# Kernel optimization log

Hardware: AMD Instinct MI355X
Metric: run time of the kernel (lower is better)

The kernel has to match this reference:

```python
import jax, jax.numpy as jnp
import numpy as np

T, N, C, S = 1600, 32, 512, 200
BLANK = 0
ALPHA = 0.5
NEG = -1e30  # finite stand-in for -inf (safe for grads)


def setup_inputs() -> dict:
    key = jax.random.key(0)
    k1, k2, k3 = jax.random.split(key, 3)
    # valid log-probabilities (log-softmax over vocab), shape (T, N, C)
    log_probs = jax.nn.log_softmax(jax.random.normal(k1, (T, N, C), jnp.float32), axis=-1)
    # labels in [1, C) so blank=0 never appears in targets
    targets = jax.random.randint(k2, (N, S), 1, C)
    input_lens = jnp.full((N,), T, dtype=jnp.int32)
    target_lens = jax.random.randint(k3, (N,), S // 2, S + 1)
    return {"log_probs": log_probs, "targets": targets,
            "input_lens": input_lens, "target_lens": target_lens}


def _ctc_forward(log_probs, targets, input_lens, target_lens):
    """Per-example CTC negative log-likelihood (reduction='none')."""
    Tt, Nn, Cc = log_probs.shape
    Ss = targets.shape[1]
    L = 2 * Ss + 1  # extended label sequence: blank, l1, blank, l2, ...

    ext = jnp.zeros((Nn, L), dtype=targets.dtype).at[:, 1::2].set(targets)  # (N, L)
    s_idx = jnp.arange(L)
    ext_m2 = jnp.pad(ext, ((0, 0), (2, 0)), constant_values=BLANK)[:, :L]
    # skip transition s-2 -> s allowed only for non-blank labels differing from s-2
    allow_skip = (ext != BLANK) & (ext != ext_m2) & (s_idx >= 2)[None, :]

    emit0 = jnp.take_along_axis(log_probs[0], ext, axis=1)  # (N, L)
    alpha0 = jnp.full((Nn, L), NEG, jnp.float32)
    alpha0 = alpha0.at[:, 0].set(emit0[:, 0])
    alpha0 = alpha0.at[:, 1].set(jnp.where(target_lens >= 1, emit0[:, 1], NEG))

    def step(alpha, xs):
        lp_t, t = xs  # lp_t: (N, C)
        emit = jnp.take_along_axis(lp_t, ext, axis=1)  # (N, L)
        a1 = jnp.pad(alpha, ((0, 0), (1, 0)), constant_values=NEG)[:, :L]
        a2 = jnp.where(allow_skip,
                       jnp.pad(alpha, ((0, 0), (2, 0)), constant_values=NEG)[:, :L],
                       NEG)
        m = jnp.maximum(jnp.maximum(alpha, a1), a2)
        new = m + jnp.log(jnp.exp(alpha - m) + jnp.exp(a1 - m) + jnp.exp(a2 - m)) + emit
        active = (t < input_lens)[:, None]  # freeze trellis past input_len
        return jnp.where(active, new, alpha), None

    alpha, _ = jax.lax.scan(step, alpha0, (log_probs[1:], jnp.arange(1, Tt)))

    idx_last = (2 * target_lens).astype(jnp.int32)  # final blank position
    idx_prev = jnp.maximum(idx_last - 1, 0)  # final label position
    a_last = jnp.take_along_axis(alpha, idx_last[:, None], axis=1)[:, 0]
    a_prev = jnp.where(target_lens > 0,
                       jnp.take_along_axis(alpha, idx_prev[:, None], axis=1)[:, 0],
                       NEG)
    return -jnp.logaddexp(a_last, a_prev)  # (N,)


def reference(log_probs, targets, input_lens, target_lens):
    per_ex = _ctc_forward(log_probs, targets, input_lens, target_lens)
    # zero_infinity=True: zero out infeasible alignments
    per_ex = jnp.where(per_ex < 1e29, per_ex, 0.0)
    norm = jnp.maximum(target_lens.astype(jnp.float32), 1.0) ** ALPHA
    return jnp.mean(per_ex / norm)
```

## Files before the change

### kernel.cpp

```cpp
#include <hip/hip_runtime.h>

#define T_DIM 1600
#define N_DIM 32
#define C_DIM 512
#define S_DIM 200
#define RCP_LN2 1.44269504088896340736f
#define LN2F 0.69314718055994530942f
#define ESENT (-(1 << 28))

static __device__ __forceinline__ float fast_exp2(float x) {
#if __has_builtin(__builtin_amdgcn_exp2f)
    return __builtin_amdgcn_exp2f(x);
#else
    return exp2f(x);
#endif
}

static __device__ __forceinline__ float fast_log2(float x) {
#if __has_builtin(__builtin_amdgcn_logf)
    return __builtin_amdgcn_logf(x);
#else
    return log2f(x);
#endif
}

static __device__ __forceinline__ float dpp_shr1_f(float x) {
    return __int_as_float(__builtin_amdgcn_update_dpp(
        0, __float_as_int(x), 0x138, 0xf, 0xf, false));
}
static __device__ __forceinline__ int dpp_shr1_i(int x, int old0) {
    return __builtin_amdgcn_update_dpp(old0, x, 0x138, 0xf, 0xf, false);
}
static __device__ __forceinline__ int dpp_prefix_max_i(int x) {
    int t;
    t = __builtin_amdgcn_update_dpp(x, x, 0x111, 0xf, 0xf, false); x = (t > x) ? t : x;
    t = __builtin_amdgcn_update_dpp(x, x, 0x112, 0xf, 0xf, false); x = (t > x) ? t : x;
    t = __builtin_amdgcn_update_dpp(x, x, 0x114, 0xf, 0xf, false); x = (t > x) ? t : x;
    t = __builtin_amdgcn_update_dpp(x, x, 0x118, 0xf, 0xf, false); x = (t > x) ? t : x;
    t = __builtin_amdgcn_update_dpp(x, x, 0x142, 0xf, 0xf, false); x = (t > x) ? t : x;
    t = __builtin_amdgcn_update_dpp(x, x, 0x143, 0xf, 0xf, false); x = (t > x) ? t : x;
    return x;
}

static __device__ __forceinline__ void gl_lds16(const float* g, float* l) {
    __builtin_amdgcn_global_load_lds(
        (const __attribute__((address_space(1))) unsigned int*)g,
        (__attribute__((address_space(3))) unsigned int*)l, 16, 0, 0);
}

#define VMWAIT8()  __builtin_amdgcn_s_waitcnt(0x0F78)
#define VMDRAIN()  __builtin_amdgcn_s_waitcnt(0x0F70)
#define PHASE_SYNC() do {                                                     \
        __builtin_amdgcn_sched_barrier(0);                                    \
        __builtin_amdgcn_s_waitcnt(0xC07F);              \
        __builtin_amdgcn_s_barrier();                                         \
        __builtin_amdgcn_sched_barrier(0);                                    \
    } while (0)

__global__ __launch_bounds__(192) void ctc_dp(
    const float* __restrict__ lp, const int* __restrict__ tgts,
    const int* __restrict__ input_lens, const int* __restrict__ target_lens,
    float* __restrict__ out, float* __restrict__ ws)
{
    __shared__ float rows[3][8][C_DIM];
    __shared__ float slab[2][5][8][64];

    const int blk = blockIdx.x;
    const int n = blk >> 1;
    const int role = blk & 1;
    const int tid = threadIdx.x;
    const int wid = tid >> 6;
    const int lane = tid & 63;
    const int* tgt = tgts + n * S_DIM;

    int len = input_lens[n];
    if (len > T_DIM) len = T_DIM;
    const int lenc = (len < 1) ? 1 : len;
    const int tl = target_lens[n];
    const int mid = (lenc + 1) >> 1;
    const int nsb = lenc - mid;
    const int nsteps = (role == 0) ? mid : nsb;
    const int nc = (nsteps + 7) >> 3;

    float* afin_g = ws + 64 + (size_t)n * 1152;
    float* bfin_g = afin_g + 512;
    int* escF_g = (int*)(afin_g + 1024);
    int* escB_g = escF_g + 64;
    int* counter = (int*)ws + n;

    int lab[4];
    float skh[4];
    if (role == 0) {
#pragma unroll
        for (int jj = 0; jj < 4; ++jj) {
            int s = lane * 8 + 2 * jj + 1;
            int i = (s - 1) >> 1;
            int lb = 0;
            float al = 0.0f;
            if (i < S_DIM) {
                lb = tgt[i];
                if (s >= 3 && i >= 1) al = (tgt[i] != tgt[i - 1]) ? 1.0f : 0.0f;
            }
            if (lb < 0 || lb >= C_DIM) lb = 0;
            lab[jj] = lb;
            skh[jj] = al;
        }
    } else {
#pragma unroll
        for (int jj = 0; jj < 4; ++jj) {
            int shat = lane * 8 + 2 * jj + 1;
            int s = 510 - shat;
            int lb = 0;
            float al = 0.0f;
            if (s >= 1 && s <= 399) {
                lb = tgt[(s - 1) >> 1];
                if (s + 2 <= 400) al = (tgt[(s + 1) >> 1] != tgt[(s - 1) >> 1]) ? 1.0f : 0.0f;
            }
            if (lb < 0 || lb >= C_DIM) lb = 0;
            lab[jj] = lb;
            skh[jj] = al;
        }
    }

    const int r0 = (wid == 1) ? 0 : 4;

    auto tmap = [&](int ti) -> int {
        if (role == 0) return ti > mid - 1 ? mid - 1 : ti;
        int t = lenc - 1 - ti;
        return t < 0 ? 0 : t;
    };

#define STAGE(B_, c_) do {                                                    \
        _Pragma("unroll")                                                     \
        for (int rr_ = 0; rr_ < 4; ++rr_) {                                   \
            int r_ = r0 + rr_;                                                \
            int t_ = tmap((c_) * 8 + r_);                                     \
            const float* g_ = lp + ((size_t)t_ * N_DIM + n) * C_DIM + lane*4; \
            gl_lds16(g_,       &rows[(B_)][r_][0]);                           \
            gl_lds16(g_ + 256, &rows[(B_)][r_][256]);                         \
        }                                                                     \
    } while (0)

#define CONV(B_, S_) do {                                                     \
        float v_[20];                                                         \
        _Pragma("unroll")                                                     \
        for (int rr_ = 0; rr_ < 4; ++rr_) {                                   \
            int r_ = r0 + rr_;                                                \
            v_[rr_ * 5 + 0] = rows[(B_)][r_][0];                              \
            v_[rr_ * 5 + 1] = rows[(B_)][r_][lab[0]];                         \
            v_[rr_ * 5 + 2] = rows[(B_)][r_][lab[1]];                         \
            v_[rr_ * 5 + 3] = rows[(B_)][r_][lab[2]];                         \
            v_[rr_ * 5 + 4] = rows[(B_)][r_][lab[3]];                         \
        }                                                                     \
        __builtin_amdgcn_sched_barrier(0);                                    \
        _Pragma("unroll")                                                     \
        for (int rr_ = 0; rr_ < 4; ++rr_) {                                   \
            int r_ = r0 + rr_;                                                \
            _Pragma("unroll")                                                 \
            for (int j_ = 0; j_ < 5; ++j_)                                    \
                slab[(S_)][j_][r_][lane] =                                    \
                    fast_exp2(v_[rr_ * 5 + j_] * RCP_LN2);                    \
        }                                                                     \
    } while (0)

#define BOUNDARY() do {                                                       \
        float lm_ = fmaxf(fmaxf(fmaxf(a0, a1), fmaxf(a2, a3)),                \
                          fmaxf(fmaxf(a4, a5), fmaxf(a6, a7)));               \
        bool nz_ = (lm_ > 0.0f);                                              \
        int kl_ = (int)((__float_as_uint(lm_) >> 23) & 0xffu) - 127;          \
        int prop_ = nz_ ? (E + kl_) : ESENT;                                  \
        int g_ = dpp_prefix_max_i(prop_ + 32 * lane);                         \
        int Efin_ = g_ - 32 * lane;                                           \
        if (nz_) {                                                            \
            int sh_ = E - Efin_;                                              \
            int h1_ = sh_ / 2, h2_ = sh_ - h1_;                               \
            float f_ = fast_exp2((float)h1_), gg_ = fast_exp2((float)h2_);    \
            float fg_ = f_ * gg_;                                             \
            a0 *= fg_; a1 *= fg_; a2 *= fg_; a3 *= fg_;                       \
            a4 *= fg_; a5 *= fg_; a6 *= fg_; a7 *= fg_;                       \
        }                                                                     \
        int Eprev_ = dpp_shr1_i(Efin_, ESENT);                                \
        E = Efin_;                                                            \
        if (lane == 0) {                                                      \
            scale_d = 0.0f;                                                   \
        } else {                                                              \
            int d_ = Eprev_ - Efin_;               \
            scale_d = (d_ < -126) ? 0.0f : fast_exp2((float)d_);              \
        }                                                                     \
    } while (0)

#define CONSUME_F(c8_, S_, FIRST_) do {                                       \
        float q_[40];                                                         \
        _Pragma("unroll")                                                     \
        for (int r_ = 0; r_ < 8; ++r_)                                        \
            _Pragma("unroll")                                                 \
            for (int j_ = 0; j_ < 5; ++j_)                                    \
                q_[r_ * 5 + j_] = slab[(S_)][j_][r_][lane];                   \
        __builtin_amdgcn_sched_barrier(0);                                    \
        _Pragma("unroll")                                                     \
        for (int r_ = 0; r_ < 8; ++r_) {                                      \
            int t_ = (c8_) + r_;                                              \
            if (t_ >= mid) break;                                             \
            float pb_ = q_[r_ * 5 + 0];                                       \
            float p1_ = q_[r_ * 5 + 1];                                       \
            float p3_ = q_[r_ * 5 + 2];                                       \
            float p5_ = q_[r_ * 5 + 3];                                       \
            float p7_ = q_[r_ * 5 + 4];                                       \
            if ((FIRST_) && r_ == 0) {                                        \
                if (lane == 0) {                                              \
                    a0 = pb_;                                                 \
                    a1 = (tl >= 1) ? p1_ : 0.0f;                              \
                }                                                             \
            } else {                                                          \
                float P_ = dpp_shr1_f(a7) * scale_d;                          \
                float n0_ = (a0 + P_) * pb_;                                  \
                float n1_ = fmaf(skh[0], P_,  a1 + a0) * p1_;                 \
                float n2_ = (a2 + a1) * pb_;                                  \
                float n3_ = fmaf(skh[1], a1, a3 + a2) * p3_;                  \
                float n4_ = (a4 + a3) * pb_;                                  \
                float n5_ = fmaf(skh[2], a3, a5 + a4) * p5_;                  \
                float n6_ = (a6 + a5) * pb_;                                  \
                float n7_ = fmaf(skh[3], a5, a7 + a6) * p7_;                  \
                a0 = n0_; a1 = n1_; a2 = n2_; a3 = n3_;                       \
                a4 = n4_; a5 = n5_; a6 = n6_; a7 = n7_;                       \
            }                                                                 \
        }                                                                     \
    } while (0)

#define CONSUME_B(c8_, S_) do {                                               \
        float q_[40];                                                         \
        _Pragma("unroll")                                                     \
        for (int r_ = 0; r_ < 8; ++r_)                                        \
            _Pragma("unroll")                                                 \
            for (int j_ = 0; j_ < 5; ++j_)                                    \
                q_[r_ * 5 + j_] = slab[(S_)][j_][r_][lane];                   \
        __builtin_amdgcn_sched_barrier(0);                                    \
        _Pragma("unroll")                                                     \
        for (int r_ = 0; r_ < 8; ++r_) {                                      \
            int ti_ = (c8_) + r_;                                             \
            if (ti_ >= nsb) break;                                            \
            float pb_ = q_[r_ * 5 + 0];                                       \
            float p1_ = q_[r_ * 5 + 1];                                       \
            float p3_ = q_[r_ * 5 + 2];                                       \
            float p5_ = q_[r_ * 5 + 3];                                       \
            float p7_ = q_[r_ * 5 + 4];                                       \
            float c0_ = pb_ * a0, c1_ = p1_ * a1;                             \
            float c2_ = pb_ * a2, c3_ = p3_ * a3;                             \
            float c4_ = pb_ * a4, c5_ = p5_ * a5;                             \
            float c6_ = pb_ * a6, c7_ = p7_ * a7;                             \
            float P_ = dpp_shr1_f(c7_) * scale_d;                             \
            a0 = c0_ + P_;                                                    \
            a1 = fmaf(skh[0], P_,  c1_ + c0_);                                \
            a2 = c2_ + c1_;                                                   \
            a3 = fmaf(skh[1], c1_, c3_ + c2_);                                \
            a4 = c4_ + c3_;                                                   \
            a5 = fmaf(skh[2], c3_, c5_ + c4_);                                \
            a6 = c6_ + c5_;                                                   \
            a7 = fmaf(skh[3], c5_, c7_ + c6_);                                \
        }                                                                     \
    } while (0)

    if (wid >= 1) {
        STAGE(0, 0);
        STAGE(1, 1);
        VMWAIT8();
        CONV(0, 0);
        STAGE(2, 2);
    }
    PHASE_SYNC();

    float a0, a1, a2, a3, a4, a5, a6, a7;
    if (role == 0) {
        a0 = a1 = a2 = a3 = a4 = a5 = a6 = a7 = 0.0f;
    } else {
#define BINIT(aj_, j_) do {                                                   \
            int s_ = 510 - (lane * 8 + (j_));                                 \
            aj_ = (s_ == 2 * tl || (tl > 0 && s_ == 2 * tl - 1)) ? 1.0f : 0.0f; \
        } while (0)
        BINIT(a0, 0); BINIT(a1, 1); BINIT(a2, 2); BINIT(a3, 3);
        BINIT(a4, 4); BINIT(a5, 5); BINIT(a6, 6); BINIT(a7, 7);
#undef BINIT
    }
    int E = 0;
    float scale_d = (lane == 0) ? 0.0f : 1.0f;

    int bg = 1, bi = 0, sw = 1, sr = 0;
    for (int k = 0; k < nc; ++k) {
        if (wid >= 1) {
            VMWAIT8();
            CONV(bg, sw);
            STAGE(bi, k + 3);
        } else {
            if (role == 0) { CONSUME_F(k * 8, sr, (k == 0)); }
            else           { CONSUME_B(k * 8, sr); }
            BOUNDARY();
        }
        PHASE_SYNC();
        bg = (bg == 2) ? 0 : bg + 1;
        bi = (bi == 2) ? 0 : bi + 1;
        sw ^= 1;
        sr ^= 1;
    }

    if (wid >= 1) {
        VMDRAIN();
        return;
    }

    {
        float4 lo = make_float4(a0, a1, a2, a3);
        float4 hi = make_float4(a4, a5, a6, a7);
        if (role == 0) {
            reinterpret_cast<float4*>(afin_g)[lane * 2] = lo;
            reinterpret_cast<float4*>(afin_g)[lane * 2 + 1] = hi;
            escF_g[lane] = E;
        } else {
            reinterpret_cast<float4*>(bfin_g)[lane * 2] = lo;
            reinterpret_cast<float4*>(bfin_g)[lane * 2 + 1] = hi;
            escB_g[lane] = E;
        }
    }

    __threadfence();
    int prev = 0;
    if (lane == 0)
        prev = __hip_atomic_fetch_add(counter, 1, __ATOMIC_ACQ_REL,
                                      __HIP_MEMORY_SCOPE_AGENT);
    prev = __shfl(prev, 0);
    if (prev != 1) return;

    __threadfence();

    {
        const int l = lane;
        const int Ef = escF_g[l];
        float m8 = -1e30f, s8 = 0.0f;
#pragma unroll
        for (int j = 0; j < 8; ++j) {
            int s = 8 * l + j;
            float x = -1e30f;
            if (s <= 400) {
                float af = afin_g[s];
                int shat = 510 - s;
                float bf = bfin_g[shat];
                if (af > 0.0f && bf > 0.0f)
                    x = fast_log2(af) + fast_log2(bf) + (float)(Ef + escB_g[shat >> 3]);
            }
            float m2 = fmaxf(m8, x);
            s8 = s8 * fast_exp2(m8 - m2) + fast_exp2(x - m2);
            m8 = m2;
        }
        float M = m8, V = s8;
#pragma unroll
        for (int off = 1; off < 64; off <<= 1) {
            float Mo = __shfl_xor(M, off);
            float Vo = __shfl_xor(V, off);
            float Mn = fmaxf(M, Mo);
            V = V * fast_exp2(M - Mn) + Vo * fast_exp2(Mo - Mn);
            M = Mn;
        }
        if (l == 0) {
            float X = M + fast_log2(V);
            float per_ex = -LN2F * X;
            if (!(per_ex < 1e29f)) per_ex = 0.0f;
            float tlf = (float)tl;
            if (tlf < 1.0f) tlf = 1.0f;
            atomicAdd(out, per_ex / sqrtf(tlf) * (1.0f / N_DIM));
        }
    }
#undef STAGE
#undef CONV
#undef BOUNDARY
#undef CONSUME_F
#undef CONSUME_B
}

extern "C" void kernel_launch(void* const* d_in, const int* in_sizes, int n_in,
                              void* d_out, int out_size, void* d_ws, size_t ws_size,
                              hipStream_t stream) {
    (void)in_sizes; (void)n_in; (void)ws_size;
    const float* lp   = (const float*)d_in[0];
    const int* tgts   = (const int*)d_in[1];
    const int* ilens  = (const int*)d_in[2];
    const int* tlens  = (const int*)d_in[3];

    hipMemsetAsync(d_out, 0, (size_t)out_size * sizeof(float), stream);
    hipMemsetAsync(d_ws, 0, N_DIM * sizeof(int), stream);
    ctc_dp<<<2 * N_DIM, 192, 0, stream>>>(lp, tgts, ilens, tlens,
                                          (float*)d_out, (float*)d_ws);
}
```

Before: 230.2 us.

## Split CTC into wide-parallel emission pack kernel plus single-wave DP kernel

Adds a pre-pass kernel, spread over 1024 blocks, that gathers each example's label emissions from every timestep row, exponentiates them, and writes a compact per-(n,t) packed array plus blank probabilities to workspace. The DP kernel then runs as a single wave per role, reading 16-byte packed emissions directly into registers with double-buffered prefetch instead of staging full 512-wide rows through LDS with producer waves and barriers. This takes the gather and exp work off the serial recurrence's critical path. The cost is a second launch and an extra round trip of the packed data through global memory. The old kernel is kept as a fallback when the workspace is too small.

```diff
diff --git a/kernel.cpp b/kernel.cpp
--- a/kernel.cpp
+++ b/kernel.cpp
@@ -27,6 +27,10 @@
 static __device__ __forceinline__ float dpp_shr1_f(float x) {
     return __int_as_float(__builtin_amdgcn_update_dpp(
         0, __float_as_int(x), 0x138, 0xf, 0xf, false));
+}
+static __device__ __forceinline__ float dpp_shl1_f(float x) {
+    return __int_as_float(__builtin_amdgcn_update_dpp(
+        0, __float_as_int(x), 0x130, 0xf, 0xf, false));
 }
 static __device__ __forceinline__ int dpp_shr1_i(int x, int old0) {
     return __builtin_amdgcn_update_dpp(old0, x, 0x138, 0xf, 0xf, false);
@@ -48,29 +52,85 @@
         (__attribute__((address_space(3))) unsigned int*)l, 16, 0, 0);
 }
 
+#define VMWAIT2()  __builtin_amdgcn_s_waitcnt(0x0F72)
 #define VMWAIT8()  __builtin_amdgcn_s_waitcnt(0x0F78)
+#define VMWAIT16() __builtin_amdgcn_s_waitcnt(0x4F70)
 #define VMDRAIN()  __builtin_amdgcn_s_waitcnt(0x0F70)
-#define PHASE_SYNC() do {                                                     \
-        __builtin_amdgcn_sched_barrier(0);                                    \
-        __builtin_amdgcn_s_waitcnt(0xC07F);              \
-        __builtin_amdgcn_s_barrier();                                         \
-        __builtin_amdgcn_sched_barrier(0);                                    \
-    } while (0)
-
-__global__ __launch_bounds__(192) void ctc_dp(
+#define SCHED0()   __builtin_amdgcn_sched_barrier(0)
+
+#define WS_COUNT_F    64
+#define WS_FIN_F      (N_DIM * 1152)
+#define WS_PBL_OFF    (WS_COUNT_F + WS_FIN_F)
+#define WS_PBL_F      (N_DIM * T_DIM + 256)
+#define WS_PACKED_OFF (WS_PBL_OFF + WS_PBL_F)
+#define WS_PACKED_F   ((size_t)N_DIM * T_DIM * 256)
+#define WS_NEED_BYTES (((size_t)WS_PACKED_OFF + WS_PACKED_F) * 4)
+
+__global__ __launch_bounds__(256) void ctc_pack(
     const float* __restrict__ lp, const int* __restrict__ tgts,
+    float* __restrict__ packed, float* __restrict__ pblank)
+{
+    __shared__ float slab[4][2][C_DIM];
+
+    const int wslot = threadIdx.x >> 6;
+    const int lane = threadIdx.x & 63;
+    const int wv = blockIdx.x * 4 + wslot;
+    const int n = wv >> 7;
+    const int w128 = wv & 127;
+    const int* tgt = tgts + n * S_DIM;
+
+    int l0 = 0, l1 = 0, l2 = 0, l3 = 0;
+    if (lane < 50) {
+        int4 li = reinterpret_cast<const int4*>(tgt)[lane];
+        l0 = li.x; l1 = li.y; l2 = li.z; l3 = li.w;
+    }
+    if (l0 < 0 || l0 >= C_DIM) l0 = 0;
+    if (l1 < 0 || l1 >= C_DIM) l1 = 0;
+    if (l2 < 0 || l2 >= C_DIM) l2 = 0;
+    if (l3 < 0 || l3 >= C_DIM) l3 = 0;
+
+    float* sl0 = &slab[wslot][0][0];
+    float* sl1 = &slab[wslot][1][0];
+    const int nj = (T_DIM - 1 - w128) / 128 + 1;
+
+    {
+        const float* g = lp + ((size_t)w128 * N_DIM + n) * C_DIM + lane * 4;
+        gl_lds16(g, sl0); gl_lds16(g + 256, sl0 + 256);
+    }
+    for (int j = 0; j < nj; ++j) {
+        const int t = w128 + 128 * j;
+        int tn = t + 128; if (tn >= T_DIM) tn = t;
+        float* snx = (j & 1) ? sl0 : sl1;
+        const float* gn = lp + ((size_t)tn * N_DIM + n) * C_DIM + lane * 4;
+        gl_lds16(gn, snx); gl_lds16(gn + 256, snx + 256);
+        VMWAIT2();
+        SCHED0();
+        const float* s = (j & 1) ? sl1 : sl0;
+        float pb = s[0];
+        float v0 = s[l0], v1 = s[l1], v2 = s[l2], v3 = s[l3];
+        float4 o;
+        o.x = fast_exp2(v0 * RCP_LN2);
+        o.y = fast_exp2(v1 * RCP_LN2);
+        o.z = fast_exp2(v2 * RCP_LN2);
+        o.w = fast_exp2(v3 * RCP_LN2);
+        reinterpret_cast<float4*>(packed)[((size_t)n * T_DIM + t) * 64 + lane] = o;
+        if (lane == 0) pblank[n * T_DIM + t] = fast_exp2(pb * RCP_LN2);
+    }
+    VMDRAIN();
+}
+
+__global__ __launch_bounds__(64) void ctc_dp2(
+    const int* __restrict__ tgts,
     const int* __restrict__ input_lens, const int* __restrict__ target_lens,
+    const float* __restrict__ packed, const float* __restrict__ pblank,
     float* __restrict__ out, float* __restrict__ ws)
 {
-    __shared__ float rows[3][8][C_DIM];
-    __shared__ float slab[2][5][8][64];
+    __shared__ float pbl[1792];
 
     const int blk = blockIdx.x;
     const int n = blk >> 1;
     const int role = blk & 1;
-    const int tid = threadIdx.x;
-    const int wid = tid >> 6;
-    const int lane = tid & 63;
+    const int lane = threadIdx.x & 63;
     const int* tgt = tgts + n * S_DIM;
 
     int len = input_lens[n];
@@ -81,28 +141,23 @@
     const int nsb = lenc - mid;
     const int nsteps = (role == 0) ? mid : nsb;
     const int nc = (nsteps + 7) >> 3;
-
-    float* afin_g = ws + 64 + (size_t)n * 1152;
+    const int ncx = ((nc + 1) >> 1) << 1;
+
+    float* afin_g = ws + WS_COUNT_F + (size_t)n * 1152;
     float* bfin_g = afin_g + 512;
     int* escF_g = (int*)(afin_g + 1024);
     int* escB_g = escF_g + 64;
     int* counter = (int*)ws + n;
 
-    int lab[4];
     float skh[4];
     if (role == 0) {
 #pragma unroll
         for (int jj = 0; jj < 4; ++jj) {
             int s = lane * 8 + 2 * jj + 1;
             int i = (s - 1) >> 1;
-            int lb = 0;
             float al = 0.0f;
-            if (i < S_DIM) {
-                lb = tgt[i];
-                if (s >= 3 && i >= 1) al = (tgt[i] != tgt[i - 1]) ? 1.0f : 0.0f;
-            }
-            if (lb < 0 || lb >= C_DIM) lb = 0;
-            lab[jj] = lb;
+            if (i < S_DIM && s >= 3 && i >= 1)
+                al = (tgt[i] != tgt[i - 1]) ? 1.0f : 0.0f;
             skh[jj] = al;
         }
     } else {
@@ -110,19 +165,22 @@
         for (int jj = 0; jj < 4; ++jj) {
             int shat = lane * 8 + 2 * jj + 1;
             int s = 510 - shat;
-            int lb = 0;
             float al = 0.0f;
-            if (s >= 1 && s <= 399) {
-                lb = tgt[(s - 1) >> 1];
-                if (s + 2 <= 400) al = (tgt[(s + 1) >> 1] != tgt[(s - 1) >> 1]) ? 1.0f : 0.0f;
-            }
-            if (lb < 0 || lb >= C_DIM) lb = 0;
-            lab[jj] = lb;
+            if (s >= 1 && s <= 399 && s + 2 <= 400)
+                al = (tgt[(s + 1) >> 1] != tgt[(s - 1) >> 1]) ? 1.0f : 0.0f;
             skh[jj] = al;
         }
     }
 
-    const int r0 = (wid == 1) ? 0 : 4;
+    const int qlane = (role == 0) ? lane : (63 - lane);
+    const float4* pk4 = reinterpret_cast<const float4*>(packed)
+                        + (size_t)n * T_DIM * 64;
+
+#pragma unroll
+    for (int k = 0; k < 7; ++k)
+        gl_lds16(pblank + (size_t)n * T_DIM + k * 256 + lane * 4, &pbl[k * 256]);
+    VMDRAIN();
+    SCHED0();
 
     auto tmap = [&](int ti) -> int {
         if (role == 0) return ti > mid - 1 ? mid - 1 : ti;
@@ -130,36 +188,12 @@
         return t < 0 ? 0 : t;
     };
 
-#define STAGE(B_, c_) do {                                                    \
-        _Pragma("unroll")                                                     \
-        for (int rr_ = 0; rr_ < 4; ++rr_) {                                   \
-            int r_ = r0 + rr_;                                                \
+#define LOADQ(QQ_, PQ_, c_) do {                                              \
+        _Pragma("unroll")                                                     \
+        for (int r_ = 0; r_ < 8; ++r_) {                                      \
             int t_ = tmap((c_) * 8 + r_);                                     \
-            const float* g_ = lp + ((size_t)t_ * N_DIM + n) * C_DIM + lane*4; \
-            gl_lds16(g_,       &rows[(B_)][r_][0]);                           \
-            gl_lds16(g_ + 256, &rows[(B_)][r_][256]);                         \
-        }                                                                     \
-    } while (0)
-
-#define CONV(B_, S_) do {                                                     \
-        float v_[20];                                                         \
-        _Pragma("unroll")                                                     \
-        for (int rr_ = 0; rr_ < 4; ++rr_) {                                   \
-            int r_ = r0 + rr_;                                                \
-            v_[rr_ * 5 + 0] = rows[(B_)][r_][0];                              \
-            v_[rr_ * 5 + 1] = rows[(B_)][r_][lab[0]];                         \
-            v_[rr_ * 5 + 2] = rows[(B_)][r_][lab[1]];                         \
-            v_[rr_ * 5 + 3] = rows[(B_)][r_][lab[2]];                         \
-            v_[rr_ * 5 + 4] = rows[(B_)][r_][lab[3]];                         \
-        }                                                                     \
-        __builtin_amdgcn_sched_barrier(0);                                    \
-        _Pragma("unroll")                                                     \
-        for (int rr_ = 0; rr_ < 4; ++rr_) {                                   \
-            int r_ = r0 + rr_;                                                \
-            _Pragma("unroll")                                                 \
-            for (int j_ = 0; j_ < 5; ++j_)                                    \
-                slab[(S_)][j_][r_][lane] =                                    \
-                    fast_exp2(v_[rr_ * 5 + j_] * RCP_LN2);                    \
+            QQ_[r_] = pk4[(size_t)t_ * 64 + qlane];                           \
+            PQ_[r_] = pbl[t_];                                                \
         }                                                                     \
     } while (0)
 
@@ -184,7 +218,300 @@
         if (lane == 0) {                                                      \
             scale_d = 0.0f;                                                   \
         } else {                                                              \
-            int d_ = Eprev_ - Efin_;               \
+            int d_ = Eprev_ - Efin_;                                          \
+            scale_d = (d_ < -126) ? 0.0f : fast_exp2((float)d_);              \
+        }                                                                     \
+    } while (0)
+
+#define COMPUTE_F2(c8_, FIRST_, QQ_, PQ_) do {                                \
+        _Pragma("unroll")                                                     \
+        for (int r_ = 0; r_ < 8; ++r_) {                                      \
+            int t_ = (c8_) + r_;                                              \
+            if (t_ >= mid) break;                                             \
+            float pb_ = PQ_[r_];                                              \
+            float p1_ = QQ_[r_].x, p3_ = QQ_[r_].y,                           \
+                  p5_ = QQ_[r_].z, p7_ = QQ_[r_].w;                           \
+            if ((FIRST_) && r_ == 0) {                                        \
+                if (lane == 0) {                                              \
+                    a0 = pb_;                                                 \
+                    a1 = (tl >= 1) ? p1_ : 0.0f;                              \
+                }                                                             \
+            } else {                                                          \
+                float P_ = dpp_shr1_f(a7) * scale_d;                          \
+                float n0_ = (a0 + P_) * pb_;                                  \
+                float n1_ = fmaf(skh[0], P_,  a1 + a0) * p1_;                 \
+                float n2_ = (a2 + a1) * pb_;                                  \
+                float n3_ = fmaf(skh[1], a1, a3 + a2) * p3_;                  \
+                float n4_ = (a4 + a3) * pb_;                                  \
+                float n5_ = fmaf(skh[2], a3, a5 + a4) * p5_;                  \
+                float n6_ = (a6 + a5) * pb_;                                  \
+                float n7_ = fmaf(skh[3], a5, a7 + a6) * p7_;                  \
+                a0 = n0_; a1 = n1_; a2 = n2_; a3 = n3_;                       \
+                a4 = n4_; a5 = n5_; a6 = n6_; a7 = n7_;                       \
+            }                                                                 \
+        }                                                                     \
+    } while (0)
+
+#define COMPUTE_B2(c8_, QQ_, PQ_) do {                                        \
+        _Pragma("unroll")                                                     \
+        for (int r_ = 0; r_ < 8; ++r_) {                                      \
+            int ti_ = (c8_) + r_;                                             \
+            if (ti_ >= nsb) break;                                            \
+            float pb_ = PQ_[r_];                                              \
+            float p1_ = QQ_[r_].z, p3_ = QQ_[r_].y, p5_ = QQ_[r_].x;          \
+            float p7_ = dpp_shl1_f(QQ_[r_].w);                                \
+            float c0_ = pb_ * a0, c1_ = p1_ * a1;                             \
+            float c2_ = pb_ * a2, c3_ = p3_ * a3;                             \
+            float c4_ = pb_ * a4, c5_ = p5_ * a5;                             \
+            float c6_ = pb_ * a6, c7_ = p7_ * a7;                             \
+            float P_ = dpp_shr1_f(c7_) * scale_d;                             \
+            a0 = c0_ + P_;                                                    \
+            a1 = fmaf(skh[0], P_,  c1_ + c0_);                                \
+            a2 = c2_ + c1_;                                                   \
+            a3 = fmaf(skh[1], c1_, c3_ + c2_);                                \
+            a4 = c4_ + c3_;                                                   \
+            a5 = fmaf(skh[2], c3_, c5_ + c4_);                                \
+            a6 = c6_ + c5_;                                                   \
+            a7 = fmaf(skh[3], c5_, c7_ + c6_);                                \
+        }                                                                     \
+    } while (0)
+
+    float a0, a1, a2, a3, a4, a5, a6, a7;
+    if (role == 0) {
+        a0 = a1 = a2 = a3 = a4 = a5 = a6 = a7 = 0.0f;
+    } else {
+#define BINIT(aj_, j_) do {                                                   \
+            int s_ = 510 - (lane * 8 + (j_));                                 \
+            aj_ = (s_ == 2 * tl || (tl > 0 && s_ == 2 * tl - 1)) ? 1.0f : 0.0f; \
+        } while (0)
+        BINIT(a0, 0); BINIT(a1, 1); BINIT(a2, 2); BINIT(a3, 3);
+        BINIT(a4, 4); BINIT(a5, 5); BINIT(a6, 6); BINIT(a7, 7);
+#undef BINIT
+    }
+    int E = 0;
+    float scale_d = (lane == 0) ? 0.0f : 1.0f;
+
+    float4 qA[8], qB[8];
+    float pbA[8], pbB[8];
+    LOADQ(qA, pbA, 0);
+    LOADQ(qB, pbB, 1);
+
+    for (int k = 0; k < ncx; k += 2) {
+        VMWAIT8();
+        SCHED0();
+        if (role == 0) { COMPUTE_F2(k * 8, (k == 0), qA, pbA); }
+        else           { COMPUTE_B2(k * 8, qA, pbA); }
+        BOUNDARY();
+        LOADQ(qA, pbA, k + 2);
+        VMWAIT8();
+        SCHED0();
+        if (role == 0) { COMPUTE_F2((k + 1) * 8, false, qB, pbB); }
+        else           { COMPUTE_B2((k + 1) * 8, qB, pbB); }
+        BOUNDARY();
+        LOADQ(qB, pbB, k + 3);
+    }
+    VMDRAIN();
+
+    {
+        float4 lo = make_float4(a0, a1, a2, a3);
+        float4 hi = make_float4(a4, a5, a6, a7);
+        if (role == 0) {
+            reinterpret_cast<float4*>(afin_g)[lane * 2] = lo;
+            reinterpret_cast<float4*>(afin_g)[lane * 2 + 1] = hi;
+            escF_g[lane] = E;
+        } else {
+            reinterpret_cast<float4*>(bfin_g)[lane * 2] = lo;
+            reinterpret_cast<float4*>(bfin_g)[lane * 2 + 1] = hi;
+            escB_g[lane] = E;
+        }
+    }
+
+    __threadfence();
+    int prev = 0;
+    if (lane == 0)
+        prev = __hip_atomic_fetch_add(counter, 1, __ATOMIC_ACQ_REL,
+                                      __HIP_MEMORY_SCOPE_AGENT);
+    prev = __shfl(prev, 0);
+    if (prev != 1) return;
+    __threadfence();
+
+    {
+        const int l = lane;
+        const int Ef = escF_g[l];
+        float m8 = -1e30f, s8 = 0.0f;
+#pragma unroll
+        for (int j = 0; j < 8; ++j) {
+            int s = 8 * l + j;
+            float x = -1e30f;
+            if (s <= 400) {
+                float af = afin_g[s];
+                int shat = 510 - s;
+                float bf = bfin_g[shat];
+                if (af > 0.0f && bf > 0.0f)
+                    x = fast_log2(af) + fast_log2(bf) + (float)(Ef + escB_g[shat >> 3]);
+            }
+            float m2 = fmaxf(m8, x);
+            s8 = s8 * fast_exp2(m8 - m2) + fast_exp2(x - m2);
+            m8 = m2;
+        }
+        float M = m8, V = s8;
+#pragma unroll
+        for (int off = 1; off < 64; off <<= 1) {
+            float Mo = __shfl_xor(M, off);
+            float Vo = __shfl_xor(V, off);
+            float Mn = fmaxf(M, Mo);
+            V = V * fast_exp2(M - Mn) + Vo * fast_exp2(Mo - Mn);
+            M = Mn;
+        }
+        if (l == 0) {
+            float X = M + fast_log2(V);
+            float per_ex = -LN2F * X;
+            if (!(per_ex < 1e29f)) per_ex = 0.0f;
+            float tlf = (float)tl;
+            if (tlf < 1.0f) tlf = 1.0f;
+            atomicAdd(out, per_ex / sqrtf(tlf) * (1.0f / N_DIM));
+        }
+    }
+#undef LOADQ
+#undef BOUNDARY
+#undef COMPUTE_F2
+#undef COMPUTE_B2
+}
+
+__global__ __launch_bounds__(192) void ctc_dp_fb(
+    const float* __restrict__ lp, const int* __restrict__ tgts,
+    const int* __restrict__ input_lens, const int* __restrict__ target_lens,
+    float* __restrict__ out, float* __restrict__ ws)
+{
+    __shared__ float rows[3][8][C_DIM];
+    __shared__ float slab[2][5][8][64];
+
+#define PHASE_SYNC() do {                                                     \
+        __builtin_amdgcn_sched_barrier(0);                                    \
+        __builtin_amdgcn_s_waitcnt(0xC07F);                                   \
+        __builtin_amdgcn_s_barrier();                                         \
+        __builtin_amdgcn_sched_barrier(0);                                    \
+    } while (0)
+
+    const int blk = blockIdx.x;
+    const int n = blk >> 1;
+    const int role = blk & 1;
+    const int tid = threadIdx.x;
+    const int wid = tid >> 6;
+    const int lane = tid & 63;
+    const int* tgt = tgts + n * S_DIM;
+
+    int len = input_lens[n];
+    if (len > T_DIM) len = T_DIM;
+    const int lenc = (len < 1) ? 1 : len;
+    const int tl = target_lens[n];
+    const int mid = (lenc + 1) >> 1;
+    const int nsb = lenc - mid;
+    const int nsteps = (role == 0) ? mid : nsb;
+    const int nc = (nsteps + 7) >> 3;
+
+    float* afin_g = ws + 64 + (size_t)n * 1152;
+    float* bfin_g = afin_g + 512;
+    int* escF_g = (int*)(afin_g + 1024);
+    int* escB_g = escF_g + 64;
+    int* counter = (int*)ws + n;
+
+    int lab[4];
+    float skh[4];
+    if (role == 0) {
+#pragma unroll
+        for (int jj = 0; jj < 4; ++jj) {
+            int s = lane * 8 + 2 * jj + 1;
+            int i = (s - 1) >> 1;
+            int lb = 0;
+            float al = 0.0f;
+            if (i < S_DIM) {
+                lb = tgt[i];
+                if (s >= 3 && i >= 1) al = (tgt[i] != tgt[i - 1]) ? 1.0f : 0.0f;
+            }
+            if (lb < 0 || lb >= C_DIM) lb = 0;
+            lab[jj] = lb;
+            skh[jj] = al;
+        }
+    } else {
+#pragma unroll
+        for (int jj = 0; jj < 4; ++jj) {
+            int shat = lane * 8 + 2 * jj + 1;
+            int s = 510 - shat;
+            int lb = 0;
+            float al = 0.0f;
+            if (s >= 1 && s <= 399) {
+                lb = tgt[(s - 1) >> 1];
+                if (s + 2 <= 400) al = (tgt[(s + 1) >> 1] != tgt[(s - 1) >> 1]) ? 1.0f : 0.0f;
+            }
+            if (lb < 0 || lb >= C_DIM) lb = 0;
+            lab[jj] = lb;
+            skh[jj] = al;
+        }
+    }
+
+    const int r0 = (wid == 1) ? 0 : 4;
+    auto tmap = [&](int ti) -> int {
+        if (role == 0) return ti > mid - 1 ? mid - 1 : ti;
+        int t = lenc - 1 - ti;
+        return t < 0 ? 0 : t;
+    };
+
+#define STAGE(B_, c_) do {                                                    \
+        _Pragma("unroll")                                                     \
+        for (int rr_ = 0; rr_ < 4; ++rr_) {                                   \
+            int r_ = r0 + rr_;                                                \
+            int t_ = tmap((c_) * 8 + r_);                                     \
+            const float* g_ = lp + ((size_t)t_ * N_DIM + n) * C_DIM + lane*4; \
+            gl_lds16(g_,       &rows[(B_)][r_][0]);                           \
+            gl_lds16(g_ + 256, &rows[(B_)][r_][256]);                         \
+        }                                                                     \
+    } while (0)
+
+#define CONV(B_, S_) do {                                                     \
+        float v_[20];                                                         \
+        _Pragma("unroll")                                                     \
+        for (int rr_ = 0; rr_ < 4; ++rr_) {                                   \
+            int r_ = r0 + rr_;                                                \
+            v_[rr_ * 5 + 0] = rows[(B_)][r_][0];                              \
+            v_[rr_ * 5 + 1] = rows[(B_)][r_][lab[0]];                         \
+            v_[rr_ * 5 + 2] = rows[(B_)][r_][lab[1]];                         \
+            v_[rr_ * 5 + 3] = rows[(B_)][r_][lab[2]];                         \
+            v_[rr_ * 5 + 4] = rows[(B_)][r_][lab[3]];                         \
+        }                                                                     \
+        __builtin_amdgcn_sched_barrier(0);                                    \
+        _Pragma("unroll")                                                     \
+        for (int rr_ = 0; rr_ < 4; ++rr_) {                                   \
+            int r_ = r0 + rr_;                                                \
+            _Pragma("unroll")                                                 \
+            for (int j_ = 0; j_ < 5; ++j_)                                    \
+                slab[(S_)][j_][r_][lane] =                                    \
+                    fast_exp2(v_[rr_ * 5 + j_] * RCP_LN2);                    \
+        }                                                                     \
+    } while (0)
+
+#define BOUNDARY() do {                                                       \
+        float lm_ = fmaxf(fmaxf(fmaxf(a0, a1), fmaxf(a2, a3)),                \
+                          fmaxf(fmaxf(a4, a5), fmaxf(a6, a7)));               \
+        bool nz_ = (lm_ > 0.0f);                                              \
+        int kl_ = (int)((__float_as_uint(lm_) >> 23) & 0xffu) - 127;          \
+        int prop_ = nz_ ? (E + kl_) : ESENT;                                  \
+        int g_ = dpp_prefix_max_i(prop_ + 32 * lane);                         \
+        int Efin_ = g_ - 32 * lane;                                           \
+        if (nz_) {                                                            \
+            int sh_ = E - Efin_;                                              \
+            int h1_ = sh_ / 2, h2_ = sh_ - h1_;                               \
+            float f_ = fast_exp2((float)h1_), gg_ = fast_exp2((float)h2_);    \
+            float fg_ = f_ * gg_;                                             \
+            a0 *= fg_; a1 *= fg_; a2 *= fg_; a3 *= fg_;                       \
+            a4 *= fg_; a5 *= fg_; a6 *= fg_; a7 *= fg_;                       \
+        }                                                                     \
+        int Eprev_ = dpp_shr1_i(Efin_, ESENT);                                \
+        E = Efin_;                                                            \
+        if (lane == 0) {                                                      \
+            scale_d = 0.0f;                                                   \
+        } else {                                                              \
+            int d_ = Eprev_ - Efin_;                                          \
             scale_d = (d_ < -126) ? 0.0f : fast_exp2((float)d_);              \
         }                                                                     \
     } while (0)
@@ -328,7 +655,6 @@
                                       __HIP_MEMORY_SCOPE_AGENT);
     prev = __shfl(prev, 0);
     if (prev != 1) return;
-
     __threadfence();
 
     {
@@ -373,12 +699,13 @@
 #undef BOUNDARY
 #undef CONSUME_F
 #undef CONSUME_B
+#undef PHASE_SYNC
 }
 
 extern "C" void kernel_launch(void* const* d_in, const int* in_sizes, int n_in,
                               void* d_out, int out_size, void* d_ws, size_t ws_size,
                               hipStream_t stream) {
-    (void)in_sizes; (void)n_in; (void)ws_size;
+    (void)in_sizes; (void)n_in;
     const float* lp   = (const float*)d_in[0];
     const int* tgts   = (const int*)d_in[1];
     const int* ilens  = (const int*)d_in[2];
@@ -386,6 +713,16 @@
 
     hipMemsetAsync(d_out, 0, (size_t)out_size * sizeof(float), stream);
     hipMemsetAsync(d_ws, 0, N_DIM * sizeof(int), stream);
-    ctc_dp<<<2 * N_DIM, 192, 0, stream>>>(lp, tgts, ilens, tlens,
-                                          (float*)d_out, (float*)d_ws);
-}
+
+    if (ws_size >= WS_NEED_BYTES) {
+        float* wsf = (float*)d_ws;
+        ctc_pack<<<1024, 256, 0, stream>>>(lp, tgts,
+                                           wsf + WS_PACKED_OFF, wsf + WS_PBL_OFF);
+        ctc_dp2<<<2 * N_DIM, 64, 0, stream>>>(tgts, ilens, tlens,
+                                              wsf + WS_PACKED_OFF, wsf + WS_PBL_OFF,
+                                              (float*)d_out, wsf);
+    } else {
+        ctc_dp_fb<<<2 * N_DIM, 192, 0, stream>>>(lp, tgts, ilens, tlens,
+                                                 (float*)d_out, (float*)d_ws);
+    }
+}
```

Measured after the change: 271.3 us. +17.9%, slower.

## Process 16 timesteps per barrier phase and replace output atomics with last-block reduction

Applied to the files above, without the earlier changes.

Doubles the chunk of timesteps handled per block-wide barrier, from 8 to 16. Staging moves from a 3-deep to a 2-deep buffer of 16 rows, and the consumer wave runs two 8-step groups, each followed by a boundary renormalisation. This halves the number of barrier phases on the serial DP critical path, at the cost of more LDS, more registers (an 80-float q array) and less prefetch depth. It also removes the memset of the output by having the last arriving block reduce the per-example results deterministically instead of using an atomicAdd into a pre-zeroed output.

```diff
diff --git a/kernel.cpp b/kernel.cpp
--- a/kernel.cpp
+++ b/kernel.cpp
@@ -48,8 +48,9 @@
         (__attribute__((address_space(3))) unsigned int*)l, 16, 0, 0);
 }
 
-#define VMWAIT8()  __builtin_amdgcn_s_waitcnt(0x0F78)
+#define VMWAIT16() __builtin_amdgcn_s_waitcnt(0x4F70)
 #define VMDRAIN()  __builtin_amdgcn_s_waitcnt(0x0F70)
+#define SCHED0()   __builtin_amdgcn_sched_barrier(0)
 #define PHASE_SYNC() do {                                                     \
         __builtin_amdgcn_sched_barrier(0);                                    \
         __builtin_amdgcn_s_waitcnt(0xC07F);              \
@@ -62,8 +63,8 @@
     const int* __restrict__ input_lens, const int* __restrict__ target_lens,
     float* __restrict__ out, float* __restrict__ ws)
 {
-    __shared__ float rows[3][8][C_DIM];
-    __shared__ float slab[2][5][8][64];
+    __shared__ float rows[2][16][C_DIM];
+    __shared__ float slab[2][5][16][64];
 
     const int blk = blockIdx.x;
     const int n = blk >> 1;
@@ -80,13 +81,15 @@
     const int mid = (lenc + 1) >> 1;
     const int nsb = lenc - mid;
     const int nsteps = (role == 0) ? mid : nsb;
-    const int nc = (nsteps + 7) >> 3;
-
-    float* afin_g = ws + 64 + (size_t)n * 1152;
+    const int nc = (nsteps + 15) >> 4;
+
+    float* afin_g = ws + 96 + (size_t)n * 1152;
     float* bfin_g = afin_g + 512;
     int* escF_g = (int*)(afin_g + 1024);
     int* escB_g = escF_g + 64;
     int* counter = (int*)ws + n;
+    int* arrivals = (int*)ws + 32;
+    float* res = ws + 33;
 
     int lab[4];
     float skh[4];
@@ -122,7 +125,7 @@
         }
     }
 
-    const int r0 = (wid == 1) ? 0 : 4;
+    const int r0 = (wid == 1) ? 0 : 8;
 
     auto tmap = [&](int ti) -> int {
         if (role == 0) return ti > mid - 1 ? mid - 1 : ti;
@@ -132,9 +135,9 @@
 
 #define STAGE(B_, c_) do {                                                    \
         _Pragma("unroll")                                                     \
-        for (int rr_ = 0; rr_ < 4; ++rr_) {                                   \
+        for (int rr_ = 0; rr_ < 8; ++rr_) {                                   \
             int r_ = r0 + rr_;                                                \
-            int t_ = tmap((c_) * 8 + r_);                                     \
+            int t_ = tmap((c_) * 16 + r_);                                    \
             const float* g_ = lp + ((size_t)t_ * N_DIM + n) * C_DIM + lane*4; \
             gl_lds16(g_,       &rows[(B_)][r_][0]);                           \
             gl_lds16(g_ + 256, &rows[(B_)][r_][256]);                         \
@@ -142,9 +145,9 @@
     } while (0)
 
 #define CONV(B_, S_) do {                                                     \
-        float v_[20];                                                         \
-        _Pragma("unroll")                                                     \
-        for (int rr_ = 0; rr_ < 4; ++rr_) {                                   \
+        float v_[40];                                                         \
+        _Pragma("unroll")                                                     \
+        for (int rr_ = 0; rr_ < 8; ++rr_) {                                   \
             int r_ = r0 + rr_;                                                \
             v_[rr_ * 5 + 0] = rows[(B_)][r_][0];                              \
             v_[rr_ * 5 + 1] = rows[(B_)][r_][lab[0]];                         \
@@ -154,7 +157,7 @@
         }                                                                     \
         __builtin_amdgcn_sched_barrier(0);                                    \
         _Pragma("unroll")                                                     \
-        for (int rr_ = 0; rr_ < 4; ++rr_) {                                   \
+        for (int rr_ = 0; rr_ < 8; ++rr_) {                                   \
             int r_ = r0 + rr_;                                                \
             _Pragma("unroll")                                                 \
             for (int j_ = 0; j_ < 5; ++j_)                                    \
@@ -189,23 +192,16 @@
         }                                                                     \
     } while (0)
 
-#define CONSUME_F(c8_, S_, FIRST_) do {                                       \
-        float q_[40];                                                         \
-        _Pragma("unroll")                                                     \
-        for (int r_ = 0; r_ < 8; ++r_)                                        \
-            _Pragma("unroll")                                                 \
-            for (int j_ = 0; j_ < 5; ++j_)                                    \
-                q_[r_ * 5 + j_] = slab[(S_)][j_][r_][lane];                   \
-        __builtin_amdgcn_sched_barrier(0);                                    \
+#define GROUP_F(t0_, qb_, q_, FIRST_) do {                                    \
         _Pragma("unroll")                                                     \
         for (int r_ = 0; r_ < 8; ++r_) {                                      \
-            int t_ = (c8_) + r_;                                              \
+            int t_ = (t0_) + r_;                                              \
             if (t_ >= mid) break;                                             \
-            float pb_ = q_[r_ * 5 + 0];                                       \
-            float p1_ = q_[r_ * 5 + 1];                                       \
-            float p3_ = q_[r_ * 5 + 2];                                       \
-            float p5_ = q_[r_ * 5 + 3];                                       \
-            float p7_ = q_[r_ * 5 + 4];                                       \
+            float pb_ = q_[(qb_ + r_) * 5 + 0];                               \
+            float p1_ = q_[(qb_ + r_) * 5 + 1];                               \
+            float p3_ = q_[(qb_ + r_) * 5 + 2];                               \
+            float p5_ = q_[(qb_ + r_) * 5 + 3];                               \
+            float p7_ = q_[(qb_ + r_) * 5 + 4];                               \
             if ((FIRST_) && r_ == 0) {                                        \
                 if (lane == 0) {                                              \
                     a0 = pb_;                                                 \
@@ -227,23 +223,16 @@
         }                                                                     \
     } while (0)
 
-#define CONSUME_B(c8_, S_) do {                                               \
-        float q_[40];                                                         \
-        _Pragma("unroll")                                                     \
-        for (int r_ = 0; r_ < 8; ++r_)                                        \
-            _Pragma("unroll")                                                 \
-            for (int j_ = 0; j_ < 5; ++j_)                                    \
-                q_[r_ * 5 + j_] = slab[(S_)][j_][r_][lane];                   \
-        __builtin_amdgcn_sched_barrier(0);                                    \
+#define GROUP_B(i0_, qb_, q_) do {                                            \
         _Pragma("unroll")                                                     \
         for (int r_ = 0; r_ < 8; ++r_) {                                      \
-            int ti_ = (c8_) + r_;                                             \
+            int ti_ = (i0_) + r_;                                             \
             if (ti_ >= nsb) break;                                            \
-            float pb_ = q_[r_ * 5 + 0];                                       \
-            float p1_ = q_[r_ * 5 + 1];                                       \
-            float p3_ = q_[r_ * 5 + 2];                                       \
-            float p5_ = q_[r_ * 5 + 3];                                       \
-            float p7_ = q_[r_ * 5 + 4];                                       \
+            float pb_ = q_[(qb_ + r_) * 5 + 0];                               \
+            float p1_ = q_[(qb_ + r_) * 5 + 1];                               \
+            float p3_ = q_[(qb_ + r_) * 5 + 2];                               \
+            float p5_ = q_[(qb_ + r_) * 5 + 3];                               \
+            float p7_ = q_[(qb_ + r_) * 5 + 4];                               \
             float c0_ = pb_ * a0, c1_ = p1_ * a1;                             \
             float c2_ = pb_ * a2, c3_ = p3_ * a3;                             \
             float c4_ = pb_ * a4, c5_ = p5_ * a5;                             \
@@ -260,12 +249,32 @@
         }                                                                     \
     } while (0)
 
+#define CONSUME(k_, S_, FIRST_) do {                                          \
+        float q_[80];                                                         \
+        _Pragma("unroll")                                                     \
+        for (int r_ = 0; r_ < 16; ++r_)                                       \
+            _Pragma("unroll")                                                 \
+            for (int j_ = 0; j_ < 5; ++j_)                                    \
+                q_[r_ * 5 + j_] = slab[(S_)][j_][r_][lane];                   \
+        __builtin_amdgcn_sched_barrier(0);                                    \
+        if (role == 0) {                                                      \
+            GROUP_F((k_) * 16,     0, q_, FIRST_);                            \
+            BOUNDARY();                                                       \
+            GROUP_F((k_) * 16 + 8, 8, q_, false);                             \
+            BOUNDARY();                                                       \
+        } else {                                                              \
+            GROUP_B((k_) * 16,     0, q_);                                    \
+            BOUNDARY();                                                       \
+            GROUP_B((k_) * 16 + 8, 8, q_);                                    \
+            BOUNDARY();                                                       \
+        }                                                                     \
+    } while (0)
+
     if (wid >= 1) {
         STAGE(0, 0);
         STAGE(1, 1);
-        VMWAIT8();
+        VMWAIT16();
         CONV(0, 0);
-        STAGE(2, 2);
     }
     PHASE_SYNC();
 
@@ -284,22 +293,15 @@
     int E = 0;
     float scale_d = (lane == 0) ? 0.0f : 1.0f;
 
-    int bg = 1, bi = 0, sw = 1, sr = 0;
     for (int k = 0; k < nc; ++k) {
         if (wid >= 1) {
-            VMWAIT8();
-            CONV(bg, sw);
-            STAGE(bi, k + 3);
+            VMDRAIN();
+            STAGE(k & 1, k + 2);
+            CONV((k + 1) & 1, (k + 1) & 1);
         } else {
-            if (role == 0) { CONSUME_F(k * 8, sr, (k == 0)); }
-            else           { CONSUME_B(k * 8, sr); }
-            BOUNDARY();
+            CONSUME(k, k & 1, (k == 0));
         }
         PHASE_SYNC();
-        bg = (bg == 2) ? 0 : bg + 1;
-        bi = (bi == 2) ? 0 : bi + 1;
-        sw ^= 1;
-        sr ^= 1;
     }
 
     if (wid >= 1) {
@@ -359,33 +361,46 @@
             V = V * fast_exp2(M - Mn) + Vo * fast_exp2(Mo - Mn);
             M = Mn;
         }
-        if (l == 0) {
+        int prev2 = 0;
+        if (lane == 0) {
             float X = M + fast_log2(V);
             float per_ex = -LN2F * X;
             if (!(per_ex < 1e29f)) per_ex = 0.0f;
             float tlf = (float)tl;
             if (tlf < 1.0f) tlf = 1.0f;
-            atomicAdd(out, per_ex / sqrtf(tlf) * (1.0f / N_DIM));
+            res[n] = per_ex / sqrtf(tlf) * (1.0f / N_DIM);
+            __threadfence();
+            prev2 = __hip_atomic_fetch_add(arrivals, 1, __ATOMIC_ACQ_REL,
+                                           __HIP_MEMORY_SCOPE_AGENT);
+        }
+        prev2 = __shfl(prev2, 0);
+        if (prev2 == N_DIM - 1) {
+            __threadfence();
+            float v = (lane < N_DIM) ? res[lane] : 0.0f;
+#pragma unroll
+            for (int off = 1; off < 64; off <<= 1)
+                v += __shfl_xor(v, off);
+            if (lane == 0) out[0] = v;
         }
     }
 #undef STAGE
 #undef CONV
 #undef BOUNDARY
-#undef CONSUME_F
-#undef CONSUME_B
+#undef GROUP_F
+#undef GROUP_B
+#undef CONSUME
 }
 
 extern "C" void kernel_launch(void* const* d_in, const int* in_sizes, int n_in,
                               void* d_out, int out_size, void* d_ws, size_t ws_size,
                               hipStream_t stream) {
-    (void)in_sizes; (void)n_in; (void)ws_size;
+    (void)in_sizes; (void)n_in; (void)out_size; (void)ws_size;
     const float* lp   = (const float*)d_in[0];
     const int* tgts   = (const int*)d_in[1];
     const int* ilens  = (const int*)d_in[2];
     const int* tlens  = (const int*)d_in[3];
 
-    hipMemsetAsync(d_out, 0, (size_t)out_size * sizeof(float), stream);
-    hipMemsetAsync(d_ws, 0, N_DIM * sizeof(int), stream);
+    hipMemsetAsync(d_ws, 0, 33 * sizeof(int), stream);
     ctc_dp<<<2 * N_DIM, 192, 0, stream>>>(lp, tgts, ilens, tlens,
                                           (float*)d_out, (float*)d_ws);
 }
```

New measurement: 222.0 us. -3.6%, faster.
